# Kernel optimization log

Hardware: AMD Instinct MI355X
Metric: run time of the kernel (lower is better)

Reference implementation:

```python
import jax, jax.numpy as jnp
import numpy as np

NEG_SLOPE = 0.2
EPS = 0.0  # default eps, non-trainable buffer
N_NODES = 50000
N_EDGES = 400000
D = 512  # state_dim


def setup_inputs() -> dict:
    key = jax.random.key(0)
    ks = jax.random.split(key, 8)
    x = jax.random.normal(ks[0], (N_NODES, D), dtype=jnp.float32)
    row = jax.random.randint(ks[1], (N_EDGES,), 0, N_NODES)
    col = jax.random.randint(ks[2], (N_EDGES,), 0, N_NODES)
    # remove_self_loops: guarantee no self loops at data-gen time (static shapes)
    col = jnp.where(row == col, (col + 1) % N_NODES, col)
    edge_index = jnp.stack([row, col], axis=0)  # [2, E]
    condition = jax.random.normal(ks[3], (1, 256), dtype=jnp.float32)
    scale = 1.0 / np.sqrt(256.0)
    Wk = jax.random.normal(ks[4], (256, 2 * D), dtype=jnp.float32) * scale
    W1 = jax.random.normal(ks[5], (D, 2 * D), dtype=jnp.float32) / np.sqrt(D)
    b1 = jnp.zeros((2 * D,), dtype=jnp.float32)
    W2 = jax.random.normal(ks[6], (2 * D, D), dtype=jnp.float32) / np.sqrt(2 * D)
    b2 = jnp.zeros((D,), dtype=jnp.float32)
    return {"x": x, "edge_index": edge_index, "condition": condition,
            "Wk": Wk, "W1": W1, "b1": b1, "W2": W2, "b2": b2}


def reference(x, edge_index, condition, Wk, W1, b1, W2, b2):
    row, col = edge_index[0], edge_index[1]
    key = condition @ Wk                      # [1, 2D]
    ki, kj = key[0, :D], key[0, D:]           # x_i pairs with first half, x_j with second
    x_i = x[col]                              # [E, D]
    # alpha = (cat([x_i, x_j]) * key).sum(-1) without materializing the concat
    alpha = x_i @ ki + x[row] @ kj            # [E]
    alpha = jnp.where(alpha >= 0, alpha, NEG_SLOPE * alpha)  # leaky_relu
    alpha = jax.nn.sigmoid(alpha)
    agg = jax.ops.segment_sum(x_i * alpha[:, None], row, num_segments=x.shape[0])
    out = (1.0 + EPS) * x + agg
    out = jax.nn.relu(out @ W1 + b1) @ W2 + b2  # h_Theta MLP
    return out
```

## Files before the change

### kernel.cpp

```cpp
#include <hip/hip_runtime.h>

#define D 512
#define H1 1024
#define NNODES 50000
#define NEDGES 400000
#define MPAD 50176
#define NEG_SLOPE 0.2f
#define SCAN_BLOCKS 196

typedef __attribute__((ext_vector_type(8))) short bf16x8;
typedef __attribute__((ext_vector_type(8))) unsigned short u16x8;
typedef __attribute__((ext_vector_type(4))) float f32x4;


__device__ __forceinline__ unsigned short f2bf(float f) {
  unsigned int u = __float_as_uint(f);
  unsigned int r = u + 0x7FFFu + ((u >> 16) & 1u);
  return (unsigned short)(r >> 16);
}
__device__ __forceinline__ float bf2f(unsigned short h) {
  return __uint_as_float((unsigned int)h << 16);
}

__global__ void key_kernel(const float* __restrict__ cond, const float* __restrict__ Wk,
                           float* __restrict__ key) {
  int j = blockIdx.x * blockDim.x + threadIdx.x;
  if (j >= 2 * D) return;
  float s = 0.f;
#pragma unroll 8
  for (int i = 0; i < 256; ++i) s += cond[i] * Wk[i * (2 * D) + j];
  key[j] = s;
}

__global__ void nodedot_kernel(const float* __restrict__ x, const float* __restrict__ key,
                               float* __restrict__ nki, float* __restrict__ nkj,
                               unsigned short* __restrict__ xb) {
  int wid = (blockIdx.x * blockDim.x + threadIdx.x) >> 6;
  int lane = threadIdx.x & 63;
  if (wid >= NNODES) return;
  const float4* xr = (const float4*)(x + (size_t)wid * D);
  float4 p0 = xr[2 * lane], p1 = xr[2 * lane + 1];
  const float4* kia = (const float4*)key;
  const float4* kja = (const float4*)(key + D);
  float4 q0 = kia[2 * lane], q1 = kia[2 * lane + 1];
  float4 r0 = kja[2 * lane], r1 = kja[2 * lane + 1];
  float a = p0.x * q0.x + p0.y * q0.y + p0.z * q0.z + p0.w * q0.w +
            p1.x * q1.x + p1.y * q1.y + p1.z * q1.z + p1.w * q1.w;
  float b = p0.x * r0.x + p0.y * r0.y + p0.z * r0.z + p0.w * r0.w +
            p1.x * r1.x + p1.y * r1.y + p1.z * r1.z + p1.w * r1.w;
  u16x8 h;
  h[0] = f2bf(p0.x); h[1] = f2bf(p0.y); h[2] = f2bf(p0.z); h[3] = f2bf(p0.w);
  h[4] = f2bf(p1.x); h[5] = f2bf(p1.y); h[6] = f2bf(p1.z); h[7] = f2bf(p1.w);
  *(u16x8*)(xb + (size_t)wid * D + 8 * lane) = h;
#pragma unroll
  for (int off = 32; off > 0; off >>= 1) {
    a += __shfl_xor(a, off);
    b += __shfl_xor(b, off);
  }
  if (lane == 0) { nki[wid] = a; nkj[wid] = b; }
}

__global__ void convw_kernel(const float* __restrict__ W1, const float* __restrict__ W2,
                             unsigned short* __restrict__ W1t, unsigned short* __restrict__ W2t) {
  int idx = blockIdx.x * blockDim.x + threadIdx.x;
  if (idx >= D * H1) return;
  {
    int k = idx / H1, n = idx % H1;
    size_t a = (((size_t)(n >> 7) * (D >> 3) + (k >> 3)) << 10) + ((n & 127) << 3) + (k & 7);
    W1t[a] = f2bf(W1[idx]);
  }
  {
    int k = idx / D, n = idx % D;
    size_t a = (((size_t)(n >> 7) * (H1 >> 3) + (k >> 3)) << 10) + ((n & 127) << 3) + (k & 7);
    W2t[a] = f2bf(W2[idx]);
  }
}

__global__ void zero_deg_kernel(int* __restrict__ deg) {
  int i = blockIdx.x * blockDim.x + threadIdx.x;
  if (i < NNODES) deg[i] = 0;
}

__global__ void hist_kernel(const int* __restrict__ row, int* __restrict__ deg) {
  int e = blockIdx.x * blockDim.x + threadIdx.x;
  if (e < NEDGES) atomicAdd(&deg[row[e]], 1);
}

__global__ void scan1_kernel(const int* __restrict__ deg, int* __restrict__ rowptr,
                             int* __restrict__ blktot) {
  __shared__ int s[256];
  int tid = threadIdx.x;
  int i = blockIdx.x * 256 + tid;
  int v = (i < NNODES) ? deg[i] : 0;
  s[tid] = v;
  __syncthreads();
#pragma unroll
  for (int off = 1; off < 256; off <<= 1) {
    int t = (tid >= off) ? s[tid - off] : 0;
    __syncthreads();
    s[tid] += t;
    __syncthreads();
  }
  if (i < NNODES) rowptr[i] = s[tid] - v;
  if (tid == 255) blktot[blockIdx.x] = s[255];
}

__global__ void scan2_kernel(int* __restrict__ blktot, int* __restrict__ blkoff) {
  __shared__ int s[256];
  int tid = threadIdx.x;
  int v = (tid < SCAN_BLOCKS) ? blktot[tid] : 0;
  s[tid] = v;
  __syncthreads();
#pragma unroll
  for (int off = 1; off < 256; off <<= 1) {
    int t = (tid >= off) ? s[tid - off] : 0;
    __syncthreads();
    s[tid] += t;
    __syncthreads();
  }
  if (tid < SCAN_BLOCKS) blkoff[tid] = s[tid] - v;
}

__global__ void scan3_kernel(int* __restrict__ rowptr, const int* __restrict__ blkoff,
                             int* __restrict__ cursor) {
  int i = blockIdx.x * blockDim.x + threadIdx.x;
  if (i < NNODES) {
    int v = rowptr[i] + blkoff[blockIdx.x];
    rowptr[i] = v;
    cursor[i] = v;
  }
  if (i == 0) rowptr[NNODES] = NEDGES;
}

__global__ void fill_kernel(const int* __restrict__ row, const int* __restrict__ col,
                            const float* __restrict__ nki, const float* __restrict__ nkj,
                            int* __restrict__ cursor, int* __restrict__ scol,
                            float* __restrict__ salpha) {
  int e = blockIdx.x * blockDim.x + threadIdx.x;
  if (e >= NEDGES) return;
  int r = row[e], c = col[e];
  float a = nki[c] + nkj[r];
  a = (a >= 0.f) ? a : NEG_SLOPE * a;
  float al = 1.f / (1.f + expf(-a));
  int pos = atomicAdd(&cursor[r], 1);
  scol[pos] = c;
  salpha[pos] = al;
}

__global__ __launch_bounds__(256) void agg_kernel(
    const unsigned short* __restrict__ xb, const int* __restrict__ rowptr,
    const int* __restrict__ scol, const float* __restrict__ salpha,
    unsigned short* __restrict__ Pb) {
  int n = (blockIdx.x * blockDim.x + threadIdx.x) >> 6;
  int lane = threadIdx.x & 63;
  if (n >= NNODES) return;
  int beg = rowptr[n], end = rowptr[n + 1];
  u16x8 self = *(const u16x8*)(xb + (size_t)n * D + 8 * lane);
  float sa[8], sb[8];
#pragma unroll
  for (int q = 0; q < 8; ++q) { sa[q] = bf2f(self[q]); sb[q] = 0.f; }
  int e = beg;
  for (; e + 1 < end; e += 2) {
    int c0 = scol[e], c1 = scol[e + 1];
    float al0 = salpha[e], al1 = salpha[e + 1];
    u16x8 w0 = *(const u16x8*)(xb + (size_t)c0 * D + 8 * lane);
    u16x8 w1 = *(const u16x8*)(xb + (size_t)c1 * D + 8 * lane);
#pragma unroll
    for (int q = 0; q < 8; ++q) {
      sa[q] += al0 * bf2f(w0[q]);
      sb[q] += al1 * bf2f(w1[q]);
    }
  }
  if (e < end) {
    int c0 = scol[e];
    float al0 = salpha[e];
    u16x8 w0 = *(const u16x8*)(xb + (size_t)c0 * D + 8 * lane);
#pragma unroll
    for (int q = 0; q < 8; ++q) sa[q] += al0 * bf2f(w0[q]);
  }
  u16x8 h;
#pragma unroll
  for (int q = 0; q < 8; ++q) h[q] = f2bf(sa[q] + sb[q]);
  *(u16x8*)(Pb + (((size_t)(n >> 7) * (D >> 3) + lane) << 10) + ((n & 127) << 3)) = h;
}

template <int K, bool RELU_OUT_BF16>
__global__ __launch_bounds__(256) void gemm_kernel(
    const unsigned short* __restrict__ Ag, const unsigned short* __restrict__ Bt,
    const float* __restrict__ bias, void* __restrict__ Cptr, int M_valid, int N) {
  constexpr int KC = K >> 3;
  constexpr int NSTEP = K >> 5;

  const int G = gridDim.x * gridDim.y;
  const int orig = blockIdx.y * gridDim.x + blockIdx.x;
  const int wg = (orig & 7) * (G >> 3) + (orig >> 3);
  const int bx = wg % gridDim.x;
  const int by = wg / gridDim.x;

  const int lane = threadIdx.x & 63;
  const int wave = threadIdx.x >> 6;
  const int wm = (wave >> 1) * 64;
  const int wn = (wave & 1) * 64;
  const int fr = lane & 15;
  const int kq = lane >> 4;

  const unsigned short* Abase = Ag + (size_t)by * KC * 1024 + (wm + fr) * 8 + kq * 1024;
  const unsigned short* Bbase = Bt + (size_t)bx * KC * 1024 + (wn + fr) * 8 + kq * 1024;

  f32x4 acc[4][4];
#pragma unroll
  for (int i = 0; i < 4; ++i)
#pragma unroll
    for (int j = 0; j < 4; ++j)
#pragma unroll
      for (int r = 0; r < 4; ++r) acc[i][j][r] = 0.f;

  bf16x8 a0[4], b0[4], a1[4], b1[4];

#define LOADSET(AV, BV, T)                                                 \
  {                                                                        \
    const unsigned short* ap_ = Abase + (size_t)(T) * 4096;                \
    const unsigned short* bp_ = Bbase + (size_t)(T) * 4096;                \
    _Pragma("unroll") for (int i = 0; i < 4; ++i)                          \
        AV[i] = *(const bf16x8*)(ap_ + i * 128);                           \
    _Pragma("unroll") for (int j = 0; j < 4; ++j)                          \
        BV[j] = *(const bf16x8*)(bp_ + j * 128);                           \
  }
#define MFMASET(AV, BV)                                                    \
  _Pragma("unroll") for (int i = 0; i < 4; ++i)                            \
      _Pragma("unroll") for (int j = 0; j < 4; ++j)                        \
          acc[i][j] = __builtin_amdgcn_mfma_f32_16x16x32_bf16(             \
              AV[i], BV[j], acc[i][j], 0, 0, 0);

  LOADSET(a0, b0, 0)
  for (int t = 0; t < NSTEP - 2; t += 2) {
    LOADSET(a1, b1, t + 1)
    MFMASET(a0, b0)
    LOADSET(a0, b0, t + 2)
    MFMASET(a1, b1)
  }
  LOADSET(a1, b1, NSTEP - 1)
  MFMASET(a0, b0)
  MFMASET(a1, b1)
#undef LOADSET
#undef MFMASET

  const int rg = kq * 4;
#pragma unroll
  for (int j = 0; j < 4; ++j) {
    const int gn = bx * 128 + wn + j * 16 + fr;
    const float bv = bias[gn];
#pragma unroll
    for (int i = 0; i < 4; ++i) {
#pragma unroll
      for (int r = 0; r < 4; ++r) {
        const int lrow = wm + i * 16 + rg + r;
        const int gm = by * 128 + lrow;
        float v = acc[i][j][r] + bv;
        if constexpr (RELU_OUT_BF16) {
          v = fmaxf(v, 0.f);
          size_t a = (((size_t)by * (N >> 3) + (gn >> 3)) << 10) + (lrow << 3) + (gn & 7);
          ((unsigned short*)Cptr)[a] = f2bf(v);
        } else {
          if (gm < M_valid) ((float*)Cptr)[(size_t)gm * N + gn] = v;
        }
      }
    }
  }
}

extern "C" void kernel_launch(void* const* d_in, const int* in_sizes, int n_in,
                              void* d_out, int out_size, void* d_ws, size_t ws_size,
                              hipStream_t stream) {
  const float* x    = (const float*)d_in[0];
  const int*   ei   = (const int*)d_in[1];
  const float* cond = (const float*)d_in[2];
  const float* Wk   = (const float*)d_in[3];
  const float* W1   = (const float*)d_in[4];
  const float* b1   = (const float*)d_in[5];
  const float* W2   = (const float*)d_in[6];
  const float* b2   = (const float*)d_in[7];
  float* out = (float*)d_out;

  char* ws = (char*)d_ws;
  size_t off = 0;
  auto alloc = [&](size_t b) { size_t p = off; off += (b + 255) & ~(size_t)255; return p; };
  float* key = (float*)(ws + alloc(2 * D * sizeof(float)));
  float* nki = (float*)(ws + alloc(NNODES * sizeof(float)));
  float* nkj = (float*)(ws + alloc(NNODES * sizeof(float)));
  int* deg    = (int*)(ws + alloc(NNODES * sizeof(int)));
  int* rowptr = (int*)(ws + alloc((NNODES + 1) * sizeof(int)));
  int* cursor = (int*)(ws + alloc(NNODES * sizeof(int)));
  int* blktot = (int*)(ws + alloc(SCAN_BLOCKS * sizeof(int)));
  int* blkoff = (int*)(ws + alloc(SCAN_BLOCKS * sizeof(int)));
  int* scol      = (int*)(ws + alloc(NEDGES * sizeof(int)));
  float* salpha  = (float*)(ws + alloc(NEDGES * sizeof(float)));
  unsigned short* xb  = (unsigned short*)(ws + alloc((size_t)NNODES * D * 2));
  unsigned short* W1t = (unsigned short*)(ws + alloc((size_t)H1 * D * 2));
  unsigned short* W2t = (unsigned short*)(ws + alloc((size_t)D * H1 * 2));
  unsigned short* Pb  = (unsigned short*)(ws + alloc((size_t)MPAD * D * 2));
  unsigned short* Hb  = (unsigned short*)(ws + alloc((size_t)MPAD * H1 * 2));

  const int* row = ei;
  const int* col = ei + NEDGES;

  key_kernel<<<dim3((2 * D + 255) / 256), dim3(256), 0, stream>>>(cond, Wk, key);
  nodedot_kernel<<<dim3(NNODES * 64 / 256), dim3(256), 0, stream>>>(x, key, nki, nkj, xb);
  convw_kernel<<<dim3(D * H1 / 256), dim3(256), 0, stream>>>(W1, W2, W1t, W2t);

  zero_deg_kernel<<<dim3(SCAN_BLOCKS), dim3(256), 0, stream>>>(deg);
  hist_kernel<<<dim3((NEDGES + 255) / 256), dim3(256), 0, stream>>>(row, deg);
  scan1_kernel<<<dim3(SCAN_BLOCKS), dim3(256), 0, stream>>>(deg, rowptr, blktot);
  scan2_kernel<<<dim3(1), dim3(256), 0, stream>>>(blktot, blkoff);
  scan3_kernel<<<dim3(SCAN_BLOCKS), dim3(256), 0, stream>>>(rowptr, blkoff, cursor);
  fill_kernel<<<dim3((NEDGES + 255) / 256), dim3(256), 0, stream>>>(row, col, nki, nkj,
                                                                    cursor, scol, salpha);
  agg_kernel<<<dim3(NNODES * 64 / 256 + 1), dim3(256), 0, stream>>>(xb, rowptr, scol, salpha, Pb);

  gemm_kernel<512, true><<<dim3(H1 / 128, MPAD / 128), dim3(256), 0, stream>>>(
      Pb, W1t, b1, Hb, NNODES, H1);
  gemm_kernel<1024, false><<<dim3(D / 128, MPAD / 128), dim3(256), 0, stream>>>(
      Hb, W2t, b2, out, NNODES, D);
}
```

Before: 394.7 us.

## Make GEMMs persistent with B panel resident in swizzled LDS

```diff
diff --git a/kernel.cpp b/kernel.cpp
--- a/kernel.cpp
+++ b/kernel.cpp
@@ -184,89 +184,115 @@
   *(u16x8*)(Pb + (((size_t)(n >> 7) * (D >> 3) + lane) << 10) + ((n & 127) << 3)) = h;
 }
 
-template <int K, bool RELU_OUT_BF16>
-__global__ __launch_bounds__(256) void gemm_kernel(
+template <int K, int NWN, bool RELU_OUT_BF16>
+__global__ __launch_bounds__(NWN * 256) void gemm_bres(
     const unsigned short* __restrict__ Ag, const unsigned short* __restrict__ Bt,
     const float* __restrict__ bias, void* __restrict__ Cptr, int M_valid, int N) {
+  constexpr int NBLK = NWN * 32;
   constexpr int KC = K >> 3;
   constexpr int NSTEP = K >> 5;
-
-  const int G = gridDim.x * gridDim.y;
-  const int orig = blockIdx.y * gridDim.x + blockIdx.x;
-  const int wg = (orig & 7) * (G >> 3) + (orig >> 3);
-  const int bx = wg % gridDim.x;
-  const int by = wg / gridDim.x;
-
-  const int lane = threadIdx.x & 63;
-  const int wave = threadIdx.x >> 6;
-  const int wm = (wave >> 1) * 64;
-  const int wn = (wave & 1) * 64;
+  constexpr int THREADS = NWN * 256;
+  constexpr int NGRAN = NBLK * KC;
+  constexpr int NTILES = MPAD / 256;
+  __shared__ unsigned short Bs[NBLK * K];
+
+  const int bx = blockIdx.x;
+  const int by = blockIdx.y;
+  const int tid = threadIdx.x;
+  const int lane = tid & 63;
+  const int wave = tid >> 6;
+  const int wm = (wave / NWN) * 64;
+  const int wn = (wave % NWN) * 32;
   const int fr = lane & 15;
   const int kq = lane >> 4;
 
-  const unsigned short* Abase = Ag + (size_t)by * KC * 1024 + (wm + fr) * 8 + kq * 1024;
-  const unsigned short* Bbase = Bt + (size_t)bx * KC * 1024 + (wn + fr) * 8 + kq * 1024;
-
-  f32x4 acc[4][4];
+  for (int g = tid; g < NGRAN; g += THREADS) {
+    const int col = g % NBLK, kc = g / NBLK;
+    const int cg = bx * NBLK + col;
+    u16x8 v = *(const u16x8*)(Bt + (((size_t)(cg >> 7) * KC + kc) << 10) + ((cg & 127) << 3));
+    const int scol = col ^ ((col >> 3) & 3) ^ ((kc & 1) << 2);
+    *(u16x8*)&Bs[(kc * NBLK + scol) * 8] = v;
+  }
+  __syncthreads();
+
+  const unsigned short* Aw = Ag + ((wm & 127) + fr) * 8 + kq * 1024;
+  const int mrb = wm >> 7;
+
+  f32x4 acc[4][2];
 #pragma unroll
   for (int i = 0; i < 4; ++i)
 #pragma unroll
-    for (int j = 0; j < 4; ++j)
+    for (int j = 0; j < 2; ++j)
 #pragma unroll
       for (int r = 0; r < 4; ++r) acc[i][j][r] = 0.f;
 
-  bf16x8 a0[4], b0[4], a1[4], b1[4];
-
-#define LOADSET(AV, BV, T)                                                 \
-  {                                                                        \
-    const unsigned short* ap_ = Abase + (size_t)(T) * 4096;                \
-    const unsigned short* bp_ = Bbase + (size_t)(T) * 4096;                \
-    _Pragma("unroll") for (int i = 0; i < 4; ++i)                          \
-        AV[i] = *(const bf16x8*)(ap_ + i * 128);                           \
-    _Pragma("unroll") for (int j = 0; j < 4; ++j)                          \
-        BV[j] = *(const bf16x8*)(bp_ + j * 128);                           \
-  }
-#define MFMASET(AV, BV)                                                    \
-  _Pragma("unroll") for (int i = 0; i < 4; ++i)                            \
-      _Pragma("unroll") for (int j = 0; j < 4; ++j)                        \
-          acc[i][j] = __builtin_amdgcn_mfma_f32_16x16x32_bf16(             \
-              AV[i], BV[j], acc[i][j], 0, 0, 0);
-
-  LOADSET(a0, b0, 0)
-  for (int t = 0; t < NSTEP - 2; t += 2) {
-    LOADSET(a1, b1, t + 1)
-    MFMASET(a0, b0)
-    LOADSET(a0, b0, t + 2)
-    MFMASET(a1, b1)
-  }
-  LOADSET(a1, b1, NSTEP - 1)
-  MFMASET(a0, b0)
-  MFMASET(a1, b1)
-#undef LOADSET
-#undef MFMASET
-
-  const int rg = kq * 4;
-#pragma unroll
-  for (int j = 0; j < 4; ++j) {
-    const int gn = bx * 128 + wn + j * 16 + fr;
-    const float bv = bias[gn];
-#pragma unroll
-    for (int i = 0; i < 4; ++i) {
-#pragma unroll
-      for (int r = 0; r < 4; ++r) {
-        const int lrow = wm + i * 16 + rg + r;
-        const int gm = by * 128 + lrow;
-        float v = acc[i][j][r] + bv;
-        if constexpr (RELU_OUT_BF16) {
-          v = fmaxf(v, 0.f);
-          size_t a = (((size_t)by * (N >> 3) + (gn >> 3)) << 10) + (lrow << 3) + (gn & 7);
-          ((unsigned short*)Cptr)[a] = f2bf(v);
-        } else {
-          if (gm < M_valid) ((float*)Cptr)[(size_t)gm * N + gn] = v;
+  bf16x8 a0[4], a1[4], bv0[2], bv1[2];
+
+#define LOADA(AV, MT, T)                                                              \
+  {                                                                                   \
+    const unsigned short* ap_ =                                                       \
+        Aw + (((size_t)((MT) * 2 + mrb) * KC) << 10) + (T) * 4096;                    \
+    _Pragma("unroll") for (int i = 0; i < 4; ++i)                                     \
+        AV[i] = *(const bf16x8*)(ap_ + i * 128);                                      \
+  }
+#define LOADB(BV, T)                                                                  \
+  {                                                                                   \
+    _Pragma("unroll") for (int j = 0; j < 2; ++j) {                                   \
+      const int col_ = wn + j * 16 + fr;                                              \
+      const int kc_ = (T) * 4 + kq;                                                   \
+      const int scol_ = col_ ^ ((col_ >> 3) & 3) ^ ((kc_ & 1) << 2);                  \
+      BV[j] = *(const bf16x8*)&Bs[(kc_ * NBLK + scol_) * 8];                          \
+    }                                                                                 \
+  }
+#define MFMASET(AV, BV)                                                               \
+  _Pragma("unroll") for (int i = 0; i < 4; ++i)                                       \
+      _Pragma("unroll") for (int j = 0; j < 2; ++j)                                   \
+          acc[i][j] = __builtin_amdgcn_mfma_f32_16x16x32_bf16(AV[i], BV[j],           \
+                                                              acc[i][j], 0, 0, 0);
+
+  LOADA(a0, by, 0) LOADB(bv0, 0)
+  for (int mt = by; mt < NTILES; mt += 32) {
+    const int mtn = (mt + 32 < NTILES) ? mt + 32 : mt;
+#pragma unroll
+    for (int t = 0; t < NSTEP - 2; t += 2) {
+      LOADA(a1, mt, t + 1) LOADB(bv1, t + 1)
+      MFMASET(a0, bv0)
+      LOADA(a0, mt, t + 2) LOADB(bv0, t + 2)
+      MFMASET(a1, bv1)
+    }
+    LOADA(a1, mt, NSTEP - 1) LOADB(bv1, NSTEP - 1)
+    MFMASET(a0, bv0)
+    LOADA(a0, mtn, 0) LOADB(bv0, 0)
+    MFMASET(a1, bv1)
+
+    const int rg = kq * 4;
+#pragma unroll
+    for (int j = 0; j < 2; ++j) {
+      const int gn = bx * NBLK + wn + j * 16 + fr;
+      const float bvl = bias[gn];
+#pragma unroll
+      for (int i = 0; i < 4; ++i) {
+#pragma unroll
+        for (int r = 0; r < 4; ++r) {
+          const int lrow = wm + i * 16 + rg + r;
+          const int gm = mt * 256 + lrow;
+          float v = acc[i][j][r] + bvl;
+          if constexpr (RELU_OUT_BF16) {
+            v = fmaxf(v, 0.f);
+            size_t aoff = (((size_t)(gm >> 7) * (N >> 3) + (gn >> 3)) << 10) +
+                          ((gm & 127) << 3) + (gn & 7);
+            ((unsigned short*)Cptr)[aoff] = f2bf(v);
+          } else {
+            if (gm < M_valid) ((float*)Cptr)[(size_t)gm * N + gn] = v;
+          }
+          acc[i][j][r] = 0.f;
         }
       }
     }
   }
+#undef LOADA
+#undef LOADB
+#undef MFMASET
 }
 
 extern "C" void kernel_launch(void* const* d_in, const int* in_sizes, int n_in,
@@ -317,8 +343,8 @@
                                                                     cursor, scol, salpha);
   agg_kernel<<<dim3(NNODES * 64 / 256 + 1), dim3(256), 0, stream>>>(xb, rowptr, scol, salpha, Pb);
 
-  gemm_kernel<512, true><<<dim3(H1 / 128, MPAD / 128), dim3(256), 0, stream>>>(
+  gemm_bres<512, 4, true><<<dim3(8, 32), dim3(1024), 0, stream>>>(
       Pb, W1t, b1, Hb, NNODES, H1);
-  gemm_kernel<1024, false><<<dim3(D / 128, MPAD / 128), dim3(256), 0, stream>>>(
+  gemm_bres<1024, 2, false><<<dim3(8, 32), dim3(512), 0, stream>>>(
       Hb, W2t, b2, out, NNODES, D);
 }
```

After: 635.9 us. +61.1%, slower.
